# Performance work log

Hardware: AMD Instinct MI355X
Metric: run time of the kernel (lower is better)

Reference implementation:

```python
import jax, jax.numpy as jnp
import numpy as np

B, H, W, C = 4, 64, 64, 256
CK = C // 8  # f/g projection dim = 32


def setup_inputs() -> dict:
    key = jax.random.key(0)
    ks = jax.random.split(key, 4)
    x = jax.random.normal(ks[0], (B, H, W, C), dtype=jnp.float32)
    Wf = jax.random.normal(ks[1], (C, CK), dtype=jnp.float32) * (1.0 / np.sqrt(C))
    Wg = jax.random.normal(ks[2], (C, CK), dtype=jnp.float32) * (1.0 / np.sqrt(C))
    Wh = jax.random.normal(ks[3], (C, C), dtype=jnp.float32) * (1.0 / np.sqrt(C))
    bf = jnp.zeros((CK,), jnp.float32)
    bg = jnp.zeros((CK,), jnp.float32)
    bh = jnp.zeros((C,), jnp.float32)
    return {"x": x, "Wf": Wf, "bf": bf, "Wg": Wg, "bg": bg, "Wh": Wh, "bh": bh}


def reference(x, Wf, bf, Wg, bg, Wh, bh):
    b, h, w, c = x.shape
    n = h * w
    xf = x.reshape(b, n, c)  # 1x1 conv == per-pixel matmul
    f = xf @ Wf + bf         # [b, n, c/8]  (keys)
    g = xf @ Wg + bg         # [b, n, c/8]  (queries)
    hh = xf @ Wh + bh        # [b, n, c]    (values)
    # s[i,j] = g_i . f_j  (tf.matmul(g, f, transpose_b=True))
    s = jnp.einsum('bik,bjk->bij', g, f)
    beta = jax.nn.softmax(s, axis=-1)
    o = jnp.einsum('bij,bjc->bic', beta, hh)
    return x + o.reshape(b, h, w, c)
```

## Files before the change

### kernel.cpp

```cpp
#include <hip/hip_runtime.h>
#include <math.h>

#define CDIM 256
#define CKD  32
#define NPIX 4096
#define BATCH 4
#define NMACRO (NPIX / 64)

typedef __attribute__((ext_vector_type(8)))  short bf16x8;
typedef __attribute__((ext_vector_type(16))) float f32x16;

#if __has_builtin(__builtin_amdgcn_exp2f)
#define EXP2(x) __builtin_amdgcn_exp2f(x)
#else
#define EXP2(x) exp2f(x)
#endif

__device__ inline ushort f2bf(float x) {
    unsigned u = __float_as_uint(x);
    u += 0x7fffu + ((u >> 16) & 1u);
    return (ushort)(u >> 16);
}
__device__ inline unsigned packbf(float a, float b) {
    return (unsigned)f2bf(a) | ((unsigned)f2bf(b) << 16);
}
__device__ inline unsigned cvtpk(float a, float b) {
    unsigned r;
    asm("v_cvt_pk_bf16_f32 %0, %1, %2" : "=v"(r) : "v"(a), "v"(b));
    return r;
}
__device__ inline void lane32swap(unsigned &a, unsigned &b) {
    asm("v_permlane32_swap_b32 %0, %1" : "+v"(a), "+v"(b));
}

#define LDS_ASYNC16(gptr, lptr) \
  __builtin_amdgcn_global_load_lds((const __attribute__((address_space(1))) void*)(gptr), \
                                   (__attribute__((address_space(3))) void*)(lptr), 16, 0, 0)

__global__ __launch_bounds__(256) void prep_kernel(
    const float* __restrict__ Wh, const float* __restrict__ Wf,
    const float* __restrict__ Wg, ushort* __restrict__ Wt)
{
    __shared__ float ls[64 * 65];
    const int tid = threadIdx.x;
    const int bid = blockIdx.x;

    if (bid < 16) {
        const int k0 = (bid & 3) * 64, c0 = (bid >> 2) * 64;
        #pragma unroll
        for (int i = 0; i < 16; ++i) {
            int r = i * 4 + (tid >> 6), c = tid & 63;
            ls[r * 65 + c] = Wh[(k0 + r) * 256 + c0 + c];
        }
        __syncthreads();
        #pragma unroll
        for (int i = 0; i < 16; ++i) {
            int cr = i * 4 + (tid >> 6), k = tid & 63;
            Wt[(c0 + cr) * 256 + k0 + k] = f2bf(ls[k * 65 + cr]);
        }
    } else {
        const float* W = (bid == 16) ? Wf : Wg;
        const int rbase = 256 + (bid - 16) * 32;
        #pragma unroll
        for (int kh2 = 0; kh2 < 2; ++kh2) {
            __syncthreads();
            #pragma unroll
            for (int i = 0; i < 16; ++i) {
                int flat = i * 256 + tid;
                int k = flat >> 5, c = flat & 31;
                ls[c * 129 + k] = W[(kh2 * 128 + k) * 32 + c];
            }
            __syncthreads();
            #pragma unroll
            for (int i = 0; i < 16; ++i) {
                int flat = i * 256 + tid;
                int c = flat >> 7, k = flat & 127;
                Wt[(rbase + c) * 256 + kh2 * 128 + k] = f2bf(ls[c * 129 + k]);
            }
        }
    }
}

__global__ __launch_bounds__(256) void proj_kernel(
    const float*  __restrict__ x,
    const ushort* __restrict__ Wt,
    const float*  __restrict__ bfp, const float* __restrict__ bgp,
    const float*  __restrict__ bhp,
    ushort* __restrict__ fo,
    ushort* __restrict__ go,
    ushort* __restrict__ glo,
    ushort* __restrict__ ht)
{
    __shared__ ushort wls[2][1280 * 8];
    __shared__ ushort xls[2][128 * 8];

    const int tid  = threadIdx.x;
    const int w    = tid >> 6;
    const int lane = tid & 63;
    const int hl   = lane >> 5;
    const int ln   = lane & 31;
    const int bid  = blockIdx.x;
    const long long px0 = (long long)bid * 32;
    const int b    = (int)(px0 >> 12);
    const int n0   = (int)(px0 & (NPIX - 1));
    const int kt   = n0 >> 6;
    const int koff = n0 & 63;

    const int sx_px = tid >> 3, sx_j = tid & 7;
    const int sx_o = sx_j >> 1, sx_h = sx_j & 1;
    const int sx_slot = sx_o * 32 + ((sx_px + 2 * sx_o) & 31);

    #pragma unroll
    for (int i = 0; i < 5; ++i) {
        int s = i * 256 + tid;
        int n = s >> 2, o = ((s & 3) - (n >> 1)) & 3;
        LDS_ASYNC16(Wt + n * 256 + o * 8, &wls[0][s * 8]);
    }
    {
        float4 v = *(const float4*)(x + (px0 + sx_px) * CDIM + sx_j * 4);
        uint2 p; p.x = packbf(v.x, v.y); p.y = packbf(v.z, v.w);
        *(uint2*)&xls[0][sx_slot * 8 + sx_h * 4] = p;
    }

    f32x16 acc0={0,0,0,0,0,0,0,0,0,0,0,0,0,0,0,0};
    f32x16 acc1={0,0,0,0,0,0,0,0,0,0,0,0,0,0,0,0};
    f32x16 accfg={0,0,0,0,0,0,0,0,0,0,0,0,0,0,0,0};

    for (int sl = 0; sl < 8; ++sl) {
        const int cur = sl & 1;
        __syncthreads();
        if (sl + 1 < 8) {
            const int nxt = cur ^ 1;
            #pragma unroll
            for (int i = 0; i < 5; ++i) {
                int s = i * 256 + tid;
                int n = s >> 2, o = ((s & 3) - (n >> 1)) & 3;
                LDS_ASYNC16(Wt + n * 256 + (sl + 1) * 32 + o * 8, &wls[nxt][s * 8]);
            }
            float4 v = *(const float4*)(x + (px0 + sx_px) * CDIM + (sl + 1) * 32 + sx_j * 4);
            uint2 p; p.x = packbf(v.x, v.y); p.y = packbf(v.z, v.w);
            *(uint2*)&xls[nxt][sx_slot * 8 + sx_h * 4] = p;
        }

        #pragma unroll
        for (int st = 0; st < 2; ++st) {
            const int o = st * 2 + hl;
            #define LDW(n) (*(const bf16x8*)&wls[cur][((n) * 4 + (((o) + ((n) >> 1)) & 3)) * 8])
            bf16x8 xb  = *(const bf16x8*)&xls[cur][(o * 32 + ((ln + 2 * o) & 31)) * 8];
            bf16x8 wa0 = LDW(w * 64 + ln);
            bf16x8 wa1 = LDW(w * 64 + 32 + ln);
            acc0 = __builtin_amdgcn_mfma_f32_32x32x16_bf16(wa0, xb, acc0, 0, 0, 0);
            acc1 = __builtin_amdgcn_mfma_f32_32x32x16_bf16(wa1, xb, acc1, 0, 0, 0);
            if (w < 2) {
                bf16x8 wfg = LDW(256 + w * 32 + ln);
                accfg = __builtin_amdgcn_mfma_f32_32x32x16_bf16(xb, wfg, accfg, 0, 0, 0);
            }
            #undef LDW
        }
    }

    ushort* htt = ht + ((long long)(b * 64 + kt) * CDIM) * 64 + koff;
    #pragma unroll
    for (int r = 0; r < 16; ++r) {
        const int rowD = (r & 3) + 8 * (r >> 2) + 4 * hl;
        int c0 = w * 64 + rowD, c1 = c0 + 32;
        htt[(long long)c0 * 64 + ln] = f2bf(acc0[r] + bhp[c0]);
        htt[(long long)c1 * 64 + ln] = f2bf(acc1[r] + bhp[c1]);
    }
    if (w < 2) {
        const float bb = (w ? bgp : bfp)[ln];
        const float scl = w ? 1.44269504088896f : 1.0f;
        #pragma unroll
        for (int r = 0; r < 16; ++r) {
            const int rowD = (r & 3) + 8 * (r >> 2) + 4 * hl;
            float v = (accfg[r] + bb) * scl;
            ushort hi = f2bf(v);
            long long idx = (px0 + rowD) * CKD + ln;
            if (w == 0) {
                fo[idx] = hi;
            } else {
                go[idx] = hi;
                float hif = __uint_as_float(((unsigned)hi) << 16);
                glo[idx] = f2bf(v - hif);
            }
        }
    }
}

__global__ __launch_bounds__(256, 2) void attn_kernel(
    const float*  __restrict__ x,
    const ushort* __restrict__ fk,
    const ushort* __restrict__ gq,
    const ushort* __restrict__ glo,
    const ushort* __restrict__ hv,
    float* __restrict__ out,
    float* __restrict__ Opart,
    float* __restrict__ Lpart,
    int nks)
{
    __shared__ ushort hh_lds[2][2048 * 8];
    __shared__ ushort f_lds[2][256 * 8];
    __shared__ float  l_red[128];

    const int tid  = threadIdx.x;
    const int w    = tid >> 6;
    const int lane = tid & 63;
    const int hl   = lane >> 5;
    const int ln   = lane & 31;

    const int bid = blockIdx.x;
    int qt, b, ks;
    if (nks == 4) {
        const int combo = bid & 15;
        qt = bid >> 4;
        b  = combo & 3;
        ks = combo >> 2;
    } else {
        qt = bid & 31;
        b  = (bid >> 5) & 3;
        ks = bid >> 7;
    }
    const int q0  = qt * 128;
    const int kt0 = (ks * NMACRO) / nks;
    const int kt1 = ((ks + 1) * NMACRO) / nks;
    const int nmac = kt1 - kt0;

    const long long bbase = (long long)b * NPIX;
    const ushort* fbase = fk + bbase * CKD;
    const ushort* htb   = hv + (long long)b * 64 * (CDIM * 64);

    const ushort* gp  = gq  + (bbase + q0 + w * 32 + ln) * CKD;
    const ushort* glp = glo + (bbase + q0 + w * 32 + ln) * CKD;
    const bf16x8 ga0 = *(const bf16x8*)(gp + hl * 8);
    const bf16x8 ga1 = *(const bf16x8*)(gp + 16 + hl * 8);
    const bf16x8 gl0 = *(const bf16x8*)(glp + hl * 8);
    const bf16x8 gl1 = *(const bf16x8*)(glp + 16 + hl * 8);

    {
        const long long tb = (long long)kt0 * (CDIM * 64);
        #pragma unroll
        for (int i = 0; i < 8; ++i) {
            int s = i * 256 + tid;
            int c = s >> 3, j = ((s & 7) - c) & 7;
            LDS_ASYNC16(htb + tb + (long long)c * 64 + j * 8, &hh_lds[0][s * 8]);
        }
        LDS_ASYNC16(fbase + (long long)(kt0 * 64 + (tid & 63)) * CKD + (tid >> 6) * 8,
                    &f_lds[0][tid * 8]);
    }

    const f32x16 Zv = {0,0,0,0,0,0,0,0,0,0,0,0,0,0,0,0};
    f32x16 acc0={0,0,0,0,0,0,0,0,0,0,0,0,0,0,0,0};
    f32x16 acc1={0,0,0,0,0,0,0,0,0,0,0,0,0,0,0,0};
    f32x16 acc2={0,0,0,0,0,0,0,0,0,0,0,0,0,0,0,0};
    f32x16 acc3={0,0,0,0,0,0,0,0,0,0,0,0,0,0,0,0};
    f32x16 acc4={0,0,0,0,0,0,0,0,0,0,0,0,0,0,0,0};
    f32x16 acc5={0,0,0,0,0,0,0,0,0,0,0,0,0,0,0,0};
    f32x16 acc6={0,0,0,0,0,0,0,0,0,0,0,0,0,0,0,0};
    f32x16 acc7={0,0,0,0,0,0,0,0,0,0,0,0,0,0,0,0};
    float lsA = 0.f, lsB = 0.f;

    #pragma unroll 2
    for (int m = 0; m < nmac; ++m) {
        const int kt = kt0 + m;
        const int cur = m & 1;
        __syncthreads();

        if (m + 1 < nmac) {
            const int nxt = cur ^ 1;
            const long long tb = (long long)(kt + 1) * (CDIM * 64);
            #pragma unroll
            for (int i = 0; i < 8; ++i) {
                int s = i * 256 + tid;
                int c = s >> 3, j = ((s & 7) - c) & 7;
                LDS_ASYNC16(htb + tb + (long long)c * 64 + j * 8, &hh_lds[nxt][s * 8]);
            }
            LDS_ASYNC16(fbase + (long long)((kt + 1) * 64 + (tid & 63)) * CKD + (tid >> 6) * 8,
                        &f_lds[nxt][tid * 8]);
        }

        #pragma unroll
        for (int kh = 0; kh < 2; ++kh) {
            f32x16 S, T;
            {
                bf16x8 fb0 = *(const bf16x8*)&f_lds[cur][((hl)     * 64 + kh * 32 + ln) * 8];
                bf16x8 fb1 = *(const bf16x8*)&f_lds[cur][((2 + hl) * 64 + kh * 32 + ln) * 8];
                __builtin_amdgcn_s_setprio(1);
                S = __builtin_amdgcn_mfma_f32_32x32x16_bf16(fb0, ga0, Zv, 0, 0, 0);
                T = __builtin_amdgcn_mfma_f32_32x32x16_bf16(fb0, gl0, Zv, 0, 0, 0);
                S = __builtin_amdgcn_mfma_f32_32x32x16_bf16(fb1, ga1, S, 0, 0, 0);
                T = __builtin_amdgcn_mfma_f32_32x32x16_bf16(fb1, gl1, T, 0, 0, 0);
                __builtin_amdgcn_s_setprio(0);
            }

            float p[16];
            #pragma unroll
            for (int r = 0; r < 16; ++r) {
                p[r] = EXP2(S[r] + T[r]);
                if (r & 1) lsB += p[r]; else lsA += p[r];
            }
            unsigned U[8];
            #pragma unroll
            for (int m2 = 0; m2 < 8; ++m2) U[m2] = cvtpk(p[2*m2], p[2*m2+1]);

            #pragma unroll
            for (int ck = 0; ck < 2; ++ck) {
                unsigned a0 = U[4*ck + 0], a1 = U[4*ck + 1];
                unsigned a2 = U[4*ck + 2], a3 = U[4*ck + 3];
                lane32swap(a0, a2);
                lane32swap(a1, a3);
                union { unsigned i[4]; bf16x8 v; } pf;
                pf.i[0] = a0; pf.i[1] = a1; pf.i[2] = a2; pf.i[3] = a3;
                bf16x8 pa = pf.v;
                const int oct = kh * 4 + ck * 2 + hl;
                const int base0 = (ln * 8 + ((oct + ln) & 7)) * 8;
                const ushort* hbp = &hh_lds[cur][base0];
                bf16x8 hb0 = *(const bf16x8*)(hbp);
                bf16x8 hb1 = *(const bf16x8*)(hbp + 1 * 2048);
                bf16x8 hb2 = *(const bf16x8*)(hbp + 2 * 2048);
                bf16x8 hb3 = *(const bf16x8*)(hbp + 3 * 2048);
                bf16x8 hb4 = *(const bf16x8*)(hbp + 4 * 2048);
                bf16x8 hb5 = *(const bf16x8*)(hbp + 5 * 2048);
                bf16x8 hb6 = *(const bf16x8*)(hbp + 6 * 2048);
                bf16x8 hb7 = *(const bf16x8*)(hbp + 7 * 2048);
                __builtin_amdgcn_s_setprio(1);
                acc0 = __builtin_amdgcn_mfma_f32_32x32x16_bf16(pa, hb0, acc0, 0, 0, 0);
                acc1 = __builtin_amdgcn_mfma_f32_32x32x16_bf16(pa, hb1, acc1, 0, 0, 0);
                acc2 = __builtin_amdgcn_mfma_f32_32x32x16_bf16(pa, hb2, acc2, 0, 0, 0);
                acc3 = __builtin_amdgcn_mfma_f32_32x32x16_bf16(pa, hb3, acc3, 0, 0, 0);
                acc4 = __builtin_amdgcn_mfma_f32_32x32x16_bf16(pa, hb4, acc4, 0, 0, 0);
                acc5 = __builtin_amdgcn_mfma_f32_32x32x16_bf16(pa, hb5, acc5, 0, 0, 0);
                acc6 = __builtin_amdgcn_mfma_f32_32x32x16_bf16(pa, hb6, acc6, 0, 0, 0);
                acc7 = __builtin_amdgcn_mfma_f32_32x32x16_bf16(pa, hb7, acc7, 0, 0, 0);
                __builtin_amdgcn_s_setprio(0);
            }
        }
    }

    float lsum = lsA + lsB;
    lsum += __shfl_xor(lsum, 32);
    if (hl == 0) l_red[w * 32 + ln] = lsum;
    __syncthreads();

    if (Opart) {
        const long long pb = ((long long)(ks * BATCH + b) * NPIX + q0);
        if (hl == 0) __builtin_nontemporal_store(lsum, &Lpart[pb + w * 32 + ln]);
        #pragma unroll
        for (int r = 0; r < 16; ++r) {
            int rowD = (r & 3) + 8 * (r >> 2) + 4 * hl;
            int ql = w * 32 + rowD;
            long long rg = (pb + ql) * CDIM + ln;
            __builtin_nontemporal_store(acc0[r], &Opart[rg]);
            __builtin_nontemporal_store(acc1[r], &Opart[rg +  32]);
            __builtin_nontemporal_store(acc2[r], &Opart[rg +  64]);
            __builtin_nontemporal_store(acc3[r], &Opart[rg +  96]);
            __builtin_nontemporal_store(acc4[r], &Opart[rg + 128]);
            __builtin_nontemporal_store(acc5[r], &Opart[rg + 160]);
            __builtin_nontemporal_store(acc6[r], &Opart[rg + 192]);
            __builtin_nontemporal_store(acc7[r], &Opart[rg + 224]);
        }
    } else {
        #pragma unroll
        for (int r = 0; r < 16; ++r) {
            int rowD = (r & 3) + 8 * (r >> 2) + 4 * hl;
            int ql = w * 32 + rowD;
            float linv = 1.f / l_red[ql];
            long long rg = (bbase + q0 + ql) * CDIM + ln;
            out[rg]       = x[rg]       + acc0[r] * linv;
            out[rg +  32] = x[rg +  32] + acc1[r] * linv;
            out[rg +  64] = x[rg +  64] + acc2[r] * linv;
            out[rg +  96] = x[rg +  96] + acc3[r] * linv;
            out[rg + 128] = x[rg + 128] + acc4[r] * linv;
            out[rg + 160] = x[rg + 160] + acc5[r] * linv;
            out[rg + 192] = x[rg + 192] + acc6[r] * linv;
            out[rg + 224] = x[rg + 224] + acc7[r] * linv;
        }
    }
}

__global__ __launch_bounds__(256) void combine_kernel(
    const float* __restrict__ x, const float* __restrict__ Op,
    const float* __restrict__ Lp, float* __restrict__ out, int nks)
{
    const int tid = threadIdx.x, w = tid >> 6, lane = tid & 63;
    const int row = blockIdx.x * 4 + w;
    const int b = row >> 12, q = row & (NPIX - 1);

    float l = 0.f;
    for (int ks = 0; ks < nks; ++ks)
        l += Lp[(ks * BATCH + b) * NPIX + q];
    const float linv = 1.f / l;

    float4 a = {0.f, 0.f, 0.f, 0.f};
    for (int ks = 0; ks < nks; ++ks) {
        const float4 v = *(const float4*)&Op[
            (((long long)(ks * BATCH + b) * NPIX + q)) * CDIM + lane * 4];
        a.x += v.x; a.y += v.y; a.z += v.z; a.w += v.w;
    }
    const long long g = ((long long)b * NPIX + q) * CDIM + lane * 4;
    const float4 xv = *(const float4*)&x[g];
    float4 o;
    o.x = xv.x + a.x * linv;
    o.y = xv.y + a.y * linv;
    o.z = xv.z + a.z * linv;
    o.w = xv.w + a.w * linv;
    *(float4*)&out[g] = o;
}

extern "C" void kernel_launch(void* const* d_in, const int* in_sizes, int n_in,
                              void* d_out, int out_size, void* d_ws, size_t ws_size,
                              hipStream_t stream) {
    const float* x  = (const float*)d_in[0];
    const float* Wf = (const float*)d_in[1];
    const float* bf = (const float*)d_in[2];
    const float* Wg = (const float*)d_in[3];
    const float* bg = (const float*)d_in[4];
    const float* Wh = (const float*)d_in[5];
    const float* bh = (const float*)d_in[6];
    float* out = (float*)d_out;

    ushort* fbf = (ushort*)d_ws;
    ushort* gbf = fbf + BATCH * NPIX * CKD;
    ushort* glo = gbf + BATCH * NPIX * CKD;
    ushort* ht  = glo + BATCH * NPIX * CKD;
    ushort* Wt  = ht + BATCH * NPIX * CDIM;
    char*   pb  = (char*)(Wt + 320 * 256);

    const size_t base_used = (size_t)(pb - (char*)d_ws);
    float* Opart = nullptr;
    float* Lpart = nullptr;
    int nks = 1;
    for (int cand = 4; cand >= 3; --cand) {
        size_t oe = (size_t)cand * BATCH * NPIX * CDIM;
        size_t le = (size_t)cand * BATCH * NPIX;
        if (ws_size >= base_used + (oe + le) * sizeof(float)) {
            nks = cand;
            Opart = (float*)pb;
            Lpart = Opart + oe;
            break;
        }
    }

    prep_kernel<<<dim3(18), 256, 0, stream>>>(Wh, Wf, Wg, Wt);
    proj_kernel<<<dim3(512), 256, 0, stream>>>(x, Wt, bf, bg, bh, fbf, gbf, glo, ht);
    attn_kernel<<<dim3(128 * nks), 256, 0, stream>>>(x, fbf, gbf, glo, ht, out,
                                                     Opart, Lpart, nks);
    if (nks > 1)
        combine_kernel<<<dim3(BATCH * NPIX / 4), 256, 0, stream>>>(x, Opart, Lpart, out, nks);
}
```

Baseline: 154.9 us.

## Prepack x and weights into MFMA fragment layout; drop LDS staging in projection

Adds an xpack kernel that converts x to bf16 in an MFMA-fragment-ready layout, and has prep_kernel store weights in a matching fragment layout. The projection kernel then reads its operands straight from global memory with no LDS double buffering and no barriers, using 2 waves that each own 5 output column tiles. The goal is to remove LDS traffic and sync overhead. In exchange it adds a kernel launch plus an extra write and read of a bf16 copy of x, and it uses fewer threads per block.

```diff
diff --git a/kernel.cpp b/kernel.cpp
--- a/kernel.cpp
+++ b/kernel.cpp
@@ -37,9 +37,14 @@
   __builtin_amdgcn_global_load_lds((const __attribute__((address_space(1))) void*)(gptr), \
                                    (__attribute__((address_space(3))) void*)(lptr), 16, 0, 0)
 
+__device__ inline void wstore(ushort* __restrict__ Wf, int n, int k, ushort v) {
+    int ks = k >> 4, hl = (k >> 3) & 1, j = k & 7;
+    Wf[((ks * 320 + n) * 2 + hl) * 8 + j] = v;
+}
+
 __global__ __launch_bounds__(256) void prep_kernel(
     const float* __restrict__ Wh, const float* __restrict__ Wf,
-    const float* __restrict__ Wg, ushort* __restrict__ Wt)
+    const float* __restrict__ Wg, ushort* __restrict__ Wfr)
 {
     __shared__ float ls[64 * 65];
     const int tid = threadIdx.x;
@@ -56,7 +61,7 @@
         #pragma unroll
         for (int i = 0; i < 16; ++i) {
             int cr = i * 4 + (tid >> 6), k = tid & 63;
-            Wt[(c0 + cr) * 256 + k0 + k] = f2bf(ls[k * 65 + cr]);
+            wstore(Wfr, c0 + cr, k0 + k, f2bf(ls[k * 65 + cr]));
         }
     } else {
         const float* W = (bid == 16) ? Wf : Wg;
@@ -75,15 +80,36 @@
             for (int i = 0; i < 16; ++i) {
                 int flat = i * 256 + tid;
                 int c = flat >> 7, k = flat & 127;
-                Wt[(rbase + c) * 256 + kh2 * 128 + k] = f2bf(ls[c * 129 + k]);
-            }
-        }
-    }
-}
-
-__global__ __launch_bounds__(256) void proj_kernel(
-    const float*  __restrict__ x,
-    const ushort* __restrict__ Wt,
+                wstore(Wfr, rbase + c, kh2 * 128 + k, f2bf(ls[c * 129 + k]));
+            }
+        }
+    }
+}
+
+__global__ __launch_bounds__(256) void xpack_kernel(
+    const float* __restrict__ x, ushort* __restrict__ xp)
+{
+    const int t = threadIdx.x, bid = blockIdx.x;
+    const long long px0 = (long long)bid * 32;
+    const int px = t >> 3, sub = t & 7;
+    ushort* dst = xp + (long long)bid * 8192;
+    #pragma unroll
+    for (int it = 0; it < 4; ++it) {
+        const int k0 = it * 64 + sub * 8;
+        const float* src = x + (px0 + px) * CDIM + k0;
+        float4 v0 = *(const float4*)src;
+        float4 v1 = *(const float4*)(src + 4);
+        uint4 pk;
+        pk.x = packbf(v0.x, v0.y); pk.y = packbf(v0.z, v0.w);
+        pk.z = packbf(v1.x, v1.y); pk.w = packbf(v1.z, v1.w);
+        const int ks = k0 >> 4, hl = (k0 >> 3) & 1;
+        *(uint4*)(dst + (ks * 64 + hl * 32 + px) * 8) = pk;
+    }
+}
+
+__global__ __launch_bounds__(128) void proj_kernel(
+    const ushort* __restrict__ xp,
+    const ushort* __restrict__ Wfr,
     const float*  __restrict__ bfp, const float* __restrict__ bgp,
     const float*  __restrict__ bhp,
     ushort* __restrict__ fo,
@@ -91,71 +117,46 @@
     ushort* __restrict__ glo,
     ushort* __restrict__ ht)
 {
-    __shared__ ushort wls[2][1280 * 8];
-    __shared__ ushort xls[2][128 * 8];
-
-    const int tid  = threadIdx.x;
-    const int w    = tid >> 6;
-    const int lane = tid & 63;
-    const int hl   = lane >> 5;
-    const int ln   = lane & 31;
-    const int bid  = blockIdx.x;
+    const int tid = threadIdx.x;
+    const int w   = tid >> 6;
+    const int L   = tid & 63;
+    const int hl  = L >> 5;
+    const int ln  = L & 31;
+    const int bid = blockIdx.x;
     const long long px0 = (long long)bid * 32;
     const int b    = (int)(px0 >> 12);
     const int n0   = (int)(px0 & (NPIX - 1));
     const int kt   = n0 >> 6;
     const int koff = n0 & 63;
 
-    const int sx_px = tid >> 3, sx_j = tid & 7;
-    const int sx_o = sx_j >> 1, sx_h = sx_j & 1;
-    const int sx_slot = sx_o * 32 + ((sx_px + 2 * sx_o) & 31);
-
-    #pragma unroll
-    for (int i = 0; i < 5; ++i) {
-        int s = i * 256 + tid;
-        int n = s >> 2, o = ((s & 3) - (n >> 1)) & 3;
-        LDS_ASYNC16(Wt + n * 256 + o * 8, &wls[0][s * 8]);
-    }
-    {
-        float4 v = *(const float4*)(x + (px0 + sx_px) * CDIM + sx_j * 4);
-        uint2 p; p.x = packbf(v.x, v.y); p.y = packbf(v.z, v.w);
-        *(uint2*)&xls[0][sx_slot * 8 + sx_h * 4] = p;
-    }
-
-    f32x16 acc0={0,0,0,0,0,0,0,0,0,0,0,0,0,0,0,0};
-    f32x16 acc1={0,0,0,0,0,0,0,0,0,0,0,0,0,0,0,0};
-    f32x16 accfg={0,0,0,0,0,0,0,0,0,0,0,0,0,0,0,0};
-
-    for (int sl = 0; sl < 8; ++sl) {
-        const int cur = sl & 1;
-        __syncthreads();
-        if (sl + 1 < 8) {
-            const int nxt = cur ^ 1;
-            #pragma unroll
-            for (int i = 0; i < 5; ++i) {
-                int s = i * 256 + tid;
-                int n = s >> 2, o = ((s & 3) - (n >> 1)) & 3;
-                LDS_ASYNC16(Wt + n * 256 + (sl + 1) * 32 + o * 8, &wls[nxt][s * 8]);
-            }
-            float4 v = *(const float4*)(x + (px0 + sx_px) * CDIM + (sl + 1) * 32 + sx_j * 4);
-            uint2 p; p.x = packbf(v.x, v.y); p.y = packbf(v.z, v.w);
-            *(uint2*)&xls[nxt][sx_slot * 8 + sx_h * 4] = p;
-        }
-
-        #pragma unroll
-        for (int st = 0; st < 2; ++st) {
-            const int o = st * 2 + hl;
-            #define LDW(n) (*(const bf16x8*)&wls[cur][((n) * 4 + (((o) + ((n) >> 1)) & 3)) * 8])
-            bf16x8 xb  = *(const bf16x8*)&xls[cur][(o * 32 + ((ln + 2 * o) & 31)) * 8];
-            bf16x8 wa0 = LDW(w * 64 + ln);
-            bf16x8 wa1 = LDW(w * 64 + 32 + ln);
-            acc0 = __builtin_amdgcn_mfma_f32_32x32x16_bf16(wa0, xb, acc0, 0, 0, 0);
-            acc1 = __builtin_amdgcn_mfma_f32_32x32x16_bf16(wa1, xb, acc1, 0, 0, 0);
-            if (w < 2) {
-                bf16x8 wfg = LDW(256 + w * 32 + ln);
-                accfg = __builtin_amdgcn_mfma_f32_32x32x16_bf16(xb, wfg, accfg, 0, 0, 0);
-            }
-            #undef LDW
+    const ushort* xpt = xp + (long long)bid * 8192;
+    const int ct0 = w * 5;
+    const ushort* wbase = Wfr + ct0 * 512 + (ln * 2 + hl) * 8;
+
+    f32x16 a0={0,0,0,0,0,0,0,0,0,0,0,0,0,0,0,0};
+    f32x16 a1={0,0,0,0,0,0,0,0,0,0,0,0,0,0,0,0};
+    f32x16 a2={0,0,0,0,0,0,0,0,0,0,0,0,0,0,0,0};
+    f32x16 a3={0,0,0,0,0,0,0,0,0,0,0,0,0,0,0,0};
+    f32x16 a4={0,0,0,0,0,0,0,0,0,0,0,0,0,0,0,0};
+
+    #pragma unroll 4
+    for (int ks = 0; ks < 16; ++ks) {
+        bf16x8 xb = *(const bf16x8*)(xpt + ks * 512 + L * 8);
+        const ushort* wk = wbase + ks * 5120;
+        bf16x8 w0 = *(const bf16x8*)(wk);
+        bf16x8 w1 = *(const bf16x8*)(wk + 512);
+        bf16x8 w2 = *(const bf16x8*)(wk + 1024);
+        bf16x8 w3 = *(const bf16x8*)(wk + 1536);
+        bf16x8 w4 = *(const bf16x8*)(wk + 2048);
+        a0 = __builtin_amdgcn_mfma_f32_32x32x16_bf16(w0, xb, a0, 0, 0, 0);
+        a1 = __builtin_amdgcn_mfma_f32_32x32x16_bf16(w1, xb, a1, 0, 0, 0);
+        a2 = __builtin_amdgcn_mfma_f32_32x32x16_bf16(w2, xb, a2, 0, 0, 0);
+        if (w == 0) {
+            a3 = __builtin_amdgcn_mfma_f32_32x32x16_bf16(w3, xb, a3, 0, 0, 0);
+            a4 = __builtin_amdgcn_mfma_f32_32x32x16_bf16(w4, xb, a4, 0, 0, 0);
+        } else {
+            a3 = __builtin_amdgcn_mfma_f32_32x32x16_bf16(xb, w3, a3, 0, 0, 0);
+            a4 = __builtin_amdgcn_mfma_f32_32x32x16_bf16(xb, w4, a4, 0, 0, 0);
         }
     }
 
@@ -163,26 +164,20 @@
     #pragma unroll
     for (int r = 0; r < 16; ++r) {
         const int rowD = (r & 3) + 8 * (r >> 2) + 4 * hl;
-        int c0 = w * 64 + rowD, c1 = c0 + 32;
-        htt[(long long)c0 * 64 + ln] = f2bf(acc0[r] + bhp[c0]);
-        htt[(long long)c1 * 64 + ln] = f2bf(acc1[r] + bhp[c1]);
-    }
-    if (w < 2) {
-        const float bb = (w ? bgp : bfp)[ln];
-        const float scl = w ? 1.44269504088896f : 1.0f;
-        #pragma unroll
-        for (int r = 0; r < 16; ++r) {
-            const int rowD = (r & 3) + 8 * (r >> 2) + 4 * hl;
-            float v = (accfg[r] + bb) * scl;
+        const int cb = ct0 * 32 + rowD;
+        htt[(long long)(cb)      * 64 + ln] = f2bf(a0[r] + bhp[cb]);
+        htt[(long long)(cb + 32) * 64 + ln] = f2bf(a1[r] + bhp[cb + 32]);
+        htt[(long long)(cb + 64) * 64 + ln] = f2bf(a2[r] + bhp[cb + 64]);
+        if (w == 0) {
+            htt[(long long)(cb +  96) * 64 + ln] = f2bf(a3[r] + bhp[cb +  96]);
+            htt[(long long)(cb + 128) * 64 + ln] = f2bf(a4[r] + bhp[cb + 128]);
+        } else {
+            long long idx = (px0 + rowD) * CKD + ln;
+            fo[idx] = f2bf(a3[r] + bfp[ln]);
+            float v = (a4[r] + bgp[ln]) * 1.44269504088896f;
             ushort hi = f2bf(v);
-            long long idx = (px0 + rowD) * CKD + ln;
-            if (w == 0) {
-                fo[idx] = hi;
-            } else {
-                go[idx] = hi;
-                float hif = __uint_as_float(((unsigned)hi) << 16);
-                glo[idx] = f2bf(v - hif);
-            }
+            go[idx] = hi;
+            glo[idx] = f2bf(v - __uint_as_float(((unsigned)hi) << 16));
         }
     }
 }
@@ -422,8 +417,9 @@
     ushort* gbf = fbf + BATCH * NPIX * CKD;
     ushort* glo = gbf + BATCH * NPIX * CKD;
     ushort* ht  = glo + BATCH * NPIX * CKD;
-    ushort* Wt  = ht + BATCH * NPIX * CDIM;
-    char*   pb  = (char*)(Wt + 320 * 256);
+    ushort* Wfr = ht + BATCH * NPIX * CDIM;
+    ushort* xp  = Wfr + 320 * 256;
+    char*   pb  = (char*)(xp + (size_t)BATCH * NPIX * CDIM);
 
     const size_t base_used = (size_t)(pb - (char*)d_ws);
     float* Opart = nullptr;
@@ -440,8 +436,9 @@
         }
     }
 
-    prep_kernel<<<dim3(18), 256, 0, stream>>>(Wh, Wf, Wg, Wt);
-    proj_kernel<<<dim3(512), 256, 0, stream>>>(x, Wt, bf, bg, bh, fbf, gbf, glo, ht);
+    prep_kernel<<<dim3(18), 256, 0, stream>>>(Wh, Wf, Wg, Wfr);
+    xpack_kernel<<<dim3(512), 256, 0, stream>>>(x, xp);
+    proj_kernel<<<dim3(512), 128, 0, stream>>>(xp, Wfr, bf, bg, bh, fbf, gbf, glo, ht);
     attn_kernel<<<dim3(128 * nks), 256, 0, stream>>>(x, fbf, gbf, glo, ht, out,
                                                      Opart, Lpart, nks);
     if (nks > 1)
```

Result: slower. 164.7 us (+6.3%).

## Fuse split-K combine into attention kernel via last-block atomic counter

Applied to the files above, without the earlier changes.

Drops the separate combine kernel. Each attention block now bumps a per-(batch, query-tile) atomic counter after writing its partial O and L, and the last of the nks splits reduces the partials, normalizes, adds the residual and writes the output. This removes one kernel launch and lets the combine overlap with other attention blocks still running. In exchange it adds a thread fence and atomic, needs the counters zeroed in prep_kernel, and puts a serial reduction tail on the last block of each tile.

```diff
diff --git a/kernel.cpp b/kernel.cpp
--- a/kernel.cpp
+++ b/kernel.cpp
@@ -39,11 +39,14 @@
 
 __global__ __launch_bounds__(256) void prep_kernel(
     const float* __restrict__ Wh, const float* __restrict__ Wf,
-    const float* __restrict__ Wg, ushort* __restrict__ Wt)
+    const float* __restrict__ Wg, ushort* __restrict__ Wt,
+    int* __restrict__ cnt)
 {
     __shared__ float ls[64 * 65];
     const int tid = threadIdx.x;
     const int bid = blockIdx.x;
+
+    if (bid == 0 && cnt && tid < 128) cnt[tid] = 0;
 
     if (bid < 16) {
         const int k0 = (bid & 3) * 64, c0 = (bid >> 2) * 64;
@@ -196,11 +199,13 @@
     float* __restrict__ out,
     float* __restrict__ Opart,
     float* __restrict__ Lpart,
+    int*   __restrict__ cnt,
     int nks)
 {
     __shared__ ushort hh_lds[2][2048 * 8];
     __shared__ ushort f_lds[2][256 * 8];
     __shared__ float  l_red[128];
+    __shared__ int    lastf;
 
     const int tid  = threadIdx.x;
     const int w    = tid >> 6;
@@ -358,6 +363,36 @@
             __builtin_nontemporal_store(acc6[r], &Opart[rg + 192]);
             __builtin_nontemporal_store(acc7[r], &Opart[rg + 224]);
         }
+
+        __threadfence();
+        __syncthreads();
+        if (tid == 0)
+            lastf = (atomicAdd(&cnt[b * 32 + qt], 1) == nks - 1);
+        __syncthreads();
+        if (lastf) {
+            __threadfence();
+            for (int rr = w; rr < 128; rr += 4) {
+                const int q = q0 + rr;
+                float l = 0.f;
+                for (int k2 = 0; k2 < nks; ++k2)
+                    l += Lpart[(k2 * BATCH + b) * NPIX + q];
+                const float linv = 1.f / l;
+                float4 a = {0.f, 0.f, 0.f, 0.f};
+                for (int k2 = 0; k2 < nks; ++k2) {
+                    const float4 v = *(const float4*)&Opart[
+                        ((long long)(k2 * BATCH + b) * NPIX + q) * CDIM + lane * 4];
+                    a.x += v.x; a.y += v.y; a.z += v.z; a.w += v.w;
+                }
+                const long long g2 = (bbase + q) * CDIM + lane * 4;
+                const float4 xv = *(const float4*)&x[g2];
+                float4 o;
+                o.x = xv.x + a.x * linv;
+                o.y = xv.y + a.y * linv;
+                o.z = xv.z + a.z * linv;
+                o.w = xv.w + a.w * linv;
+                *(float4*)&out[g2] = o;
+            }
+        }
     } else {
         #pragma unroll
         for (int r = 0; r < 16; ++r) {
@@ -377,35 +412,6 @@
     }
 }
 
-__global__ __launch_bounds__(256) void combine_kernel(
-    const float* __restrict__ x, const float* __restrict__ Op,
-    const float* __restrict__ Lp, float* __restrict__ out, int nks)
-{
-    const int tid = threadIdx.x, w = tid >> 6, lane = tid & 63;
-    const int row = blockIdx.x * 4 + w;
-    const int b = row >> 12, q = row & (NPIX - 1);
-
-    float l = 0.f;
-    for (int ks = 0; ks < nks; ++ks)
-        l += Lp[(ks * BATCH + b) * NPIX + q];
-    const float linv = 1.f / l;
-
-    float4 a = {0.f, 0.f, 0.f, 0.f};
-    for (int ks = 0; ks < nks; ++ks) {
-        const float4 v = *(const float4*)&Op[
-            (((long long)(ks * BATCH + b) * NPIX + q)) * CDIM + lane * 4];
-        a.x += v.x; a.y += v.y; a.z += v.z; a.w += v.w;
-    }
-    const long long g = ((long long)b * NPIX + q) * CDIM + lane * 4;
-    const float4 xv = *(const float4*)&x[g];
-    float4 o;
-    o.x = xv.x + a.x * linv;
-    o.y = xv.y + a.y * linv;
-    o.z = xv.z + a.z * linv;
-    o.w = xv.w + a.w * linv;
-    *(float4*)&out[g] = o;
-}
-
 extern "C" void kernel_launch(void* const* d_in, const int* in_sizes, int n_in,
                               void* d_out, int out_size, void* d_ws, size_t ws_size,
                               hipStream_t stream) {
@@ -428,22 +434,22 @@
     const size_t base_used = (size_t)(pb - (char*)d_ws);
     float* Opart = nullptr;
     float* Lpart = nullptr;
+    int*   cnt   = nullptr;
     int nks = 1;
     for (int cand = 4; cand >= 3; --cand) {
         size_t oe = (size_t)cand * BATCH * NPIX * CDIM;
         size_t le = (size_t)cand * BATCH * NPIX;
-        if (ws_size >= base_used + (oe + le) * sizeof(float)) {
+        if (ws_size >= base_used + (oe + le) * sizeof(float) + 512) {
             nks = cand;
             Opart = (float*)pb;
             Lpart = Opart + oe;
+            cnt   = (int*)(Lpart + le);
             break;
         }
     }
 
-    prep_kernel<<<dim3(18), 256, 0, stream>>>(Wh, Wf, Wg, Wt);
+    prep_kernel<<<dim3(18), 256, 0, stream>>>(Wh, Wf, Wg, Wt, cnt);
     proj_kernel<<<dim3(512), 256, 0, stream>>>(x, Wt, bf, bg, bh, fbf, gbf, glo, ht);
     attn_kernel<<<dim3(128 * nks), 256, 0, stream>>>(x, fbf, gbf, glo, ht, out,
-                                                     Opart, Lpart, nks);
-    if (nks > 1)
-        combine_kernel<<<dim3(BATCH * NPIX / 4), 256, 0, stream>>>(x, Opart, Lpart, out, nks);
-}
+                                                     Opart, Lpart, cnt, nks);
+}
```

Result: slower. 342.6 us (+121.2%).
